# Kernel optimization log

Hardware: AMD Instinct MI355X
Metric: run time of the kernel (lower is better)

Reference implementation:

```python
import jax, jax.numpy as jnp
import numpy as np

EPS_INTERP = 1e-8
EPS_BN = 1e-5


def _bn_relu(x, gamma, beta):
    # x: [B, C, N]; training-mode BatchNorm1d over (B, N) with biased variance
    mean = jnp.mean(x, axis=(0, 2), keepdims=True)
    var = jnp.mean((x - mean) ** 2, axis=(0, 2), keepdims=True)
    xn = (x - mean) / jnp.sqrt(var + EPS_BN)
    return jax.nn.relu(xn * gamma[None, :, None] + beta[None, :, None])


def setup_inputs() -> dict:
    key = jax.random.key(0)
    ks = jax.random.split(key, 8)
    B, N, S, D = 16, 4096, 1024, 128
    return {
        "xyz1": jax.random.normal(ks[0], (B, 3, N), jnp.float32),
        "xyz2": jax.random.normal(ks[1], (B, 3, S), jnp.float32),
        "points1": jax.random.normal(ks[2], (B, D, N), jnp.float32),
        "points2": jax.random.normal(ks[3], (B, D, S), jnp.float32),
        "w0": jax.random.normal(ks[4], (256, 512), jnp.float32) * 0.04,
        "b0": jax.random.normal(ks[5], (256,), jnp.float32) * 0.01,
        "gamma0": jnp.ones((256,), jnp.float32),
        "beta0": jnp.zeros((256,), jnp.float32),
        "w1": jax.random.normal(ks[6], (128, 256), jnp.float32) * 0.06,
        "b1": jax.random.normal(ks[7], (128,), jnp.float32) * 0.01,
        "gamma1": jnp.ones((128,), jnp.float32),
        "beta1": jnp.zeros((128,), jnp.float32),
    }


def reference(xyz1, xyz2, points1, points2, w0, b0, gamma0, beta0, w1, b1, gamma1, beta1):
    # to [B, N, C] layouts
    x1 = jnp.transpose(xyz1, (0, 2, 1))   # [B, N, 3]
    x2 = jnp.transpose(xyz2, (0, 2, 1))   # [B, S, 3]
    p2 = jnp.transpose(points2, (0, 2, 1))  # [B, S, D]
    B, N, _ = x1.shape

    # squared pairwise distances [B, N, S]
    dists = (jnp.sum(x1 ** 2, -1)[:, :, None]
             + jnp.sum(x2 ** 2, -1)[:, None, :]
             - 2.0 * jnp.einsum('bnc,bsc->bns', x1, x2))

    # 3 nearest neighbors (ascending distance)
    neg_d, idx = jax.lax.top_k(-dists, 3)   # idx: [B, N, 3]
    d3 = -neg_d
    recip = 1.0 / (d3 + EPS_INTERP)
    weight = recip / jnp.sum(recip, axis=2, keepdims=True)  # [B, N, 3]

    # gather neighbor features: [B, N, 3, D]
    gathered = jax.vmap(lambda p, i: p[i])(p2, idx)
    # NOTE: this repo flattens the 3 weighted neighbors (no sum) -> [B, N, 3*D]
    interp = (gathered * weight[..., None]).reshape(B, N, -1)

    new_pts = jnp.concatenate([jnp.transpose(points1, (0, 2, 1)), interp], axis=-1)  # [B, N, 512]
    x = jnp.transpose(new_pts, (0, 2, 1))  # [B, 512, N]

    x = _bn_relu(jnp.einsum('oc,bcn->bon', w0, x) + b0[None, :, None], gamma0, beta0)
    x = _bn_relu(jnp.einsum('oc,bcn->bon', w1, x) + b1[None, :, None], gamma1, beta1)
    return x
```

## Files before the change

### kernel.cpp

```cpp
#include <hip/hip_runtime.h>
#include <stdint.h>

typedef unsigned short ushort_t;
typedef __attribute__((ext_vector_type(8))) __bf16 bf16x8;
typedef __attribute__((ext_vector_type(4))) float f32x4;

__device__ __forceinline__ float b2f(ushort_t u) {
    unsigned v = ((unsigned)u) << 16;
    float f;
    __builtin_memcpy(&f, &v, 4);
    return f;
}

__device__ __forceinline__ ushort_t f2b(float f) {
    __bf16 h = (__bf16)f;
    return __builtin_bit_cast(ushort_t, h);
}

__device__ __forceinline__ void gl_lds16(const void* g, void* l) {
    __builtin_amdgcn_global_load_lds((const __attribute__((address_space(1))) void*)g,
                                     (__attribute__((address_space(3))) void*)l, 16, 0, 0);
}

__global__ __launch_bounds__(256) void k_pre(const float* __restrict__ w0, ushort_t* __restrict__ w0b,
                                             const float* __restrict__ w1, ushort_t* __restrict__ w1b,
                                             const float* __restrict__ xyz2, float4* __restrict__ sdat,
                                             const float* __restrict__ points2, ushort_t* __restrict__ p2t,
                                             float* __restrict__ zb) {
    int bid = blockIdx.x;
    int t = threadIdx.x;
    if (bid < 512) {
        int i = bid * 256 + t;
        w0b[i] = f2b(w0[i]);
    } else if (bid < 640) {
        int i = (bid - 512) * 256 + t;
        w1b[i] = f2b(w1[i]);
    } else if (bid < 704) {
        int bb = bid - 640;
        int b = bb & 15, by = bb >> 4;
        int s = by * 256 + t;
        const float* x2 = xyz2 + (size_t)b * 3 * 1024;
        float x = x2[s], y = x2[1024 + s], z = x2[2048 + s];
        float4 v;
        v.x = x; v.y = y; v.z = z;
        v.w = __fadd_rn(__fadd_rn(__fmul_rn(x, x), __fmul_rn(y, y)), __fmul_rn(z, z));
        sdat[(size_t)b * 1024 + s] = v;
    } else if (bid < 960) {
        int bb = bid - 704;
        int b = bb & 15, sy = bb >> 4;
        int s = sy * 64 + (t & 63);
        int g = t >> 6;
        const float* src = points2 + (size_t)b * 128 * 1024 + s;
        ushort_t* dst = p2t + ((size_t)b * 1024 + s) * 128;
#pragma unroll
        for (int i = 0; i < 4; ++i) {
            int cp = i * 4 + g;
            ushort_t tmp[8];
#pragma unroll
            for (int k = 0; k < 8; ++k) tmp[k] = f2b(src[(size_t)(cp * 8 + k) * 1024]);
            *(uint4*)(dst + cp * 8) = *(const uint4*)tmp;
        }
    } else {
        zb[t] = 0.f; zb[256 + t] = 0.f;
        if (t < 128) { zb[512 + t] = 0.f; zb[640 + t] = 0.f; }
    }
}

__global__ __launch_bounds__(256) void k_interp(const float* __restrict__ xyz1,
                                                const float4* __restrict__ sdat,
                                                const float* __restrict__ points1,
                                                ushort_t* __restrict__ Xp1,
                                                int* __restrict__ sidxg,
                                                float* __restrict__ swg) {
    int b = blockIdx.x;
    int n0 = blockIdx.y * 32;
    int t = threadIdx.x;
    int tq = t & 31;
    int slice = t >> 5;
    int wave = t >> 6, lane = t & 63;

    __shared__ __align__(16) char sbuf[16384];
    float4* sP = (float4*)sbuf;
    __shared__ float sD[768];
    __shared__ int   sI[768];

    {
        const float4* src = sdat + (size_t)b * 1024;
#pragma unroll
        for (int c = 0; c < 4; ++c) {
            int p = wave * 256 + c * 64 + lane;
            gl_lds16(src + p, sbuf + p * 16);
        }
    }

    int n = n0 + tq;
    float x = xyz1[((size_t)b * 3 + 0) * 4096 + n];
    float y = xyz1[((size_t)b * 3 + 1) * 4096 + n];
    float z = xyz1[((size_t)b * 3 + 2) * 4096 + n];
    float s1 = __fadd_rn(__fadd_rn(__fmul_rn(x, x), __fmul_rn(y, y)), __fmul_rn(z, z));

    __syncthreads();

    const float* p1base = points1 + (size_t)b * 128 * 4096 + n0 + tq;
    float p1v[16];
#pragma unroll
    for (int i = 0; i < 2; ++i)
#pragma unroll
        for (int k = 0; k < 8; ++k)
            p1v[i * 8 + k] = p1base[(size_t)(((i * 8 + slice) * 8) + k) * 4096];

    float d0 = 1e30f, d1 = 1e30f, d2 = 1e30f;
    int i0 = 0, i1 = 0, i2 = 0;
    int sbeg = slice * 128;
    const float4* sdL = sP + sbeg;
#pragma unroll 8
    for (int s = 0; s < 128; ++s) {
        float4 v = sdL[s];
        float dot = fmaf(z, v.z, fmaf(y, v.y, __fmul_rn(x, v.x)));
        float d = __fadd_rn(fmaf(-2.0f, dot, s1), v.w);
        int si = sbeg + s;
        bool c0 = d < d0, c1 = d < d1, c2 = d < d2;
        i2 = c1 ? i1 : (c2 ? si : i2);
        i1 = c0 ? i0 : (c1 ? si : i1);
        i0 = c0 ? si : i0;
        d2 = fminf(fmaxf(d, d1), d2);
        d1 = fminf(fmaxf(d, d0), d1);
        d0 = fminf(d, d0);
    }
    sD[t * 3 + 0] = d0; sD[t * 3 + 1] = d1; sD[t * 3 + 2] = d2;
    sI[t * 3 + 0] = i0; sI[t * 3 + 1] = i1; sI[t * 3 + 2] = i2;

    {
        ushort_t* dstbase = Xp1 + (size_t)(b * 4096 + n0 + tq) * 128;
#pragma unroll
        for (int i = 0; i < 2; ++i) {
            int piece = i * 8 + slice;
            ushort_t tmp[8];
#pragma unroll
            for (int k = 0; k < 8; ++k) tmp[k] = f2b(p1v[i * 8 + k]);
            *(uint4*)(dstbase + piece * 8) = *(const uint4*)tmp;
        }
    }
    __syncthreads();

    if (t < 32) {
        int sel0 = -1, sel1 = -1;
        float seld[3]; int seli[3];
#pragma unroll
        for (int r = 0; r < 3; ++r) {
            float bd = 1e38f; int bi = 1 << 30;
            for (int k = 0; k < 24; ++k) {
                int s3 = (k * 0xAAAB) >> 17;
                int rank = k - s3 * 3;
                int base = (s3 * 32 + t) * 3 + rank;
                float cd = sD[base];
                int ci = sI[base];
                bool excl = (ci == sel0) | (ci == sel1);
                bool better = (!excl) & ((cd < bd) | ((cd == bd) & (ci < bi)));
                if (better) { bd = cd; bi = ci; }
            }
            seld[r] = bd; seli[r] = bi;
            if (r == 0) sel0 = bi; else if (r == 1) sel1 = bi;
        }
        float r0 = 1.0f / (seld[0] + 1e-8f);
        float r1 = 1.0f / (seld[1] + 1e-8f);
        float r2 = 1.0f / (seld[2] + 1e-8f);
        float rs = r0 + r1 + r2;
        size_t base = (size_t)(b * 4096 + n0 + t) * 3;
        sidxg[base + 0] = seli[0]; sidxg[base + 1] = seli[1]; sidxg[base + 2] = seli[2];
        swg[base + 0] = r0 / rs; swg[base + 1] = r1 / rs; swg[base + 2] = r2 / rs;
    }
}

__global__ __launch_bounds__(512, 4) void k_gemm(const ushort_t* __restrict__ A,
                                                 const ushort_t* __restrict__ Xp1,
                                                 const ushort_t* __restrict__ p2t,
                                                 const int* __restrict__ sidxg,
                                                 const float* __restrict__ swg,
                                                 const float* __restrict__ bias,
                                                 ushort_t* __restrict__ Y,
                                                 float* __restrict__ gs,
                                                 float* __restrict__ gq,
                                                 int Mtot, int K) {
    __shared__ __align__(16) char smem[54784];
    ushort_t* As = (ushort_t*)smem;
    ushort_t* Bs = (ushort_t*)(smem + 32768);
    ushort_t* sY = (ushort_t*)smem;
    float* red_s = (float*)(smem + 49152);
    float* red_q = red_s + 256;
    int*   lsi   = (int*)(smem + 51200);
    float* lsw   = (float*)(smem + 52736);

    int t = threadIdx.x;
    int j0 = blockIdx.x * 128;
    int b = j0 >> 12;
    int wave = t >> 6, lane = t & 63;
    int wm = wave >> 1, wn = wave & 1;
    int l16 = lane & 15, quad = lane >> 4;

    if (t < 256) { red_s[t] = 0.f; red_q[t] = 0.f; }
    if (t < 384) { lsi[t] = sidxg[(size_t)j0 * 3 + t]; lsw[t] = swg[(size_t)j0 * 3 + t]; }

    f32x4 acc[4][4] = {};

    int nk = K >> 6;
    for (int kt = 0; kt < nk; ++kt) {
#pragma unroll
        for (int c = 0; c < 4; ++c) {
            int idx = c * 512 + t;
            int row = idx >> 3, kc = idx & 7;
            gl_lds16(A + (size_t)row * K + kt * 64 + kc * 8, As + idx * 8);
        }
        if (kt < 2) {
#pragma unroll
            for (int c = 0; c < 2; ++c) {
                int idx = c * 512 + t;
                int row = idx >> 3, kc = idx & 7;
                gl_lds16(Xp1 + (size_t)(j0 + row) * 128 + kt * 64 + kc * 8, Bs + idx * 8);
            }
        } else {
            int r = (kt - 2) >> 1, h = (kt - 2) & 1;
#pragma unroll
            for (int c = 0; c < 2; ++c) {
                int idx = c * 512 + t;
                int row = idx >> 3, kc = idx & 7;
                int si = lsi[row * 3 + r];
                float w = lsw[row * 3 + r];
                const ushort_t* src = p2t + ((size_t)b * 1024 + si) * 128 + h * 64 + kc * 8;
                uint4 raw = *(const uint4*)src;
                ushort_t* e = (ushort_t*)&raw;
                ushort_t outv[8];
#pragma unroll
                for (int k = 0; k < 8; ++k) outv[k] = f2b(w * b2f(e[k]));
                *(uint4*)(Bs + idx * 8) = *(const uint4*)outv;
            }
        }
        __syncthreads();

#pragma unroll
        for (int kk = 0; kk < 2; ++kk) {
            bf16x8 af[4], bfr[4];
#pragma unroll
            for (int mi = 0; mi < 4; ++mi)
                af[mi] = *(const bf16x8*)(As + (wm * 64 + mi * 16 + l16) * 64 + kk * 32 + quad * 8);
#pragma unroll
            for (int ni = 0; ni < 4; ++ni)
                bfr[ni] = *(const bf16x8*)(Bs + (wn * 64 + ni * 16 + l16) * 64 + kk * 32 + quad * 8);
#pragma unroll
            for (int mi = 0; mi < 4; ++mi)
#pragma unroll
                for (int ni = 0; ni < 4; ++ni)
                    acc[mi][ni] = __builtin_amdgcn_mfma_f32_16x16x32_bf16(af[mi], bfr[ni], acc[mi][ni], 0, 0, 0);
        }
        __syncthreads();
    }

#pragma unroll
    for (int h = 0; h < 2; ++h) {
        if ((wm >> 1) == h) {
#pragma unroll
            for (int mi = 0; mi < 4; ++mi) {
                int obase = wm * 64 + mi * 16 + quad * 4;
                int ocol = obase - h * 128;
                float bv[4];
#pragma unroll
                for (int r = 0; r < 4; ++r) bv[r] = bias[obase + r];
                float sr[4] = {0.f, 0.f, 0.f, 0.f}, qr[4] = {0.f, 0.f, 0.f, 0.f};
#pragma unroll
                for (int ni = 0; ni < 4; ++ni) {
                    int j_local = wn * 64 + ni * 16 + l16;
                    ushort4 pk;
                    float v0 = acc[mi][ni][0] + bv[0];
                    float v1 = acc[mi][ni][1] + bv[1];
                    float v2 = acc[mi][ni][2] + bv[2];
                    float v3 = acc[mi][ni][3] + bv[3];
                    pk.x = f2b(v0); pk.y = f2b(v1); pk.z = f2b(v2); pk.w = f2b(v3);
                    sr[0] += v0; qr[0] += v0 * v0;
                    sr[1] += v1; qr[1] += v1 * v1;
                    sr[2] += v2; qr[2] += v2 * v2;
                    sr[3] += v3; qr[3] += v3 * v3;
                    *(ushort4*)(sY + j_local * 136 + ocol) = pk;
                }
#pragma unroll
                for (int r = 0; r < 4; ++r) {
                    float s = sr[r], q = qr[r];
                    s += __shfl_xor(s, 1); s += __shfl_xor(s, 2);
                    s += __shfl_xor(s, 4); s += __shfl_xor(s, 8);
                    q += __shfl_xor(q, 1); q += __shfl_xor(q, 2);
                    q += __shfl_xor(q, 4); q += __shfl_xor(q, 8);
                    if (l16 == 0) {
                        atomicAdd(&red_s[obase + r], s);
                        atomicAdd(&red_q[obase + r], q);
                    }
                }
            }
        }
        __syncthreads();
#pragma unroll
        for (int rep = 0; rep < 4; ++rep) {
            int idx = rep * 512 + t;
            int jl = idx >> 4;
            int o8 = idx & 15;
            uint4 vv = *(const uint4*)(sY + jl * 136 + o8 * 8);
            *(uint4*)(Y + (size_t)(j0 + jl) * Mtot + h * 128 + o8 * 8) = vv;
        }
        __syncthreads();
    }
    if (t < 256) {
        atomicAdd(&gs[t], red_s[t]);
        atomicAdd(&gq[t], red_q[t]);
    }
}

__global__ __launch_bounds__(256) void k_gemmf(const ushort_t* __restrict__ A,
                                               const ushort_t* __restrict__ Y0,
                                               const float* __restrict__ bias,
                                               const float* __restrict__ gamma0,
                                               const float* __restrict__ beta0,
                                               const float* __restrict__ gs0,
                                               const float* __restrict__ gq0,
                                               ushort_t* __restrict__ Y,
                                               float* __restrict__ gs1,
                                               float* __restrict__ gq1,
                                               int Mtot, int K) {
    __shared__ __align__(16) char smem[35840];
    ushort_t* As = (ushort_t*)smem;
    ushort_t* Bs = (ushort_t*)(smem + 16384);
    float* sa = (float*)(smem + 32768);
    float* sb = (float*)(smem + 33792);
    ushort_t* sY = (ushort_t*)smem;
    float* red_s = (float*)(smem + 34816);
    float* red_q = red_s + 128;

    int t = threadIdx.x;
    int m0 = blockIdx.x * 128;
    int j0 = blockIdx.y * 128;
    int wave = t >> 6, lane = t & 63;
    int wm = wave >> 1, wn = wave & 1;
    int l16 = lane & 15, quad = lane >> 4;

    {
        float s = gs0[t], q = gq0[t];
        float mean = s * (1.0f / 65536.0f);
        float var = q * (1.0f / 65536.0f) - mean * mean;
        float sc = gamma0[t] / sqrtf(var + 1e-5f);
        sa[t] = sc;
        sb[t] = beta0[t] - mean * sc;
    }
    if (t < 128) { red_s[t] = 0.f; red_q[t] = 0.f; }
    __syncthreads();

    f32x4 acc[4][4] = {};

    int nk = K >> 6;
    for (int kt = 0; kt < nk; ++kt) {
#pragma unroll
        for (int c = 0; c < 4; ++c) {
            int idx = c * 256 + t;
            int row = idx >> 3, kc = idx & 7;
            gl_lds16(A + (size_t)(m0 + row) * K + kt * 64 + kc * 8, As + idx * 8);
        }
#pragma unroll
        for (int c = 0; c < 4; ++c) {
            int idx = c * 256 + t;
            int row = idx >> 3, kc = idx & 7;
            int cbase = kt * 64 + kc * 8;
            uint4 raw = *(const uint4*)(Y0 + (size_t)(j0 + row) * K + cbase);
            ushort_t* e = (ushort_t*)&raw;
            ushort_t outv[8];
#pragma unroll
            for (int k = 0; k < 8; ++k) {
                float v = fmaxf(sa[cbase + k] * b2f(e[k]) + sb[cbase + k], 0.f);
                outv[k] = f2b(v);
            }
            *(uint4*)(Bs + idx * 8) = *(const uint4*)outv;
        }
        __syncthreads();

#pragma unroll
        for (int kk = 0; kk < 2; ++kk) {
            bf16x8 af[4], bfr[4];
#pragma unroll
            for (int mi = 0; mi < 4; ++mi)
                af[mi] = *(const bf16x8*)(As + (wm * 64 + mi * 16 + l16) * 64 + kk * 32 + quad * 8);
#pragma unroll
            for (int ni = 0; ni < 4; ++ni)
                bfr[ni] = *(const bf16x8*)(Bs + (wn * 64 + ni * 16 + l16) * 64 + kk * 32 + quad * 8);
#pragma unroll
            for (int mi = 0; mi < 4; ++mi)
#pragma unroll
                for (int ni = 0; ni < 4; ++ni)
                    acc[mi][ni] = __builtin_amdgcn_mfma_f32_16x16x32_bf16(af[mi], bfr[ni], acc[mi][ni], 0, 0, 0);
        }
        __syncthreads();
    }

#pragma unroll
    for (int mi = 0; mi < 4; ++mi) {
        int obase = wm * 64 + mi * 16 + quad * 4;
        float bv[4];
#pragma unroll
        for (int r = 0; r < 4; ++r) bv[r] = bias[m0 + obase + r];
        float sr[4] = {0.f, 0.f, 0.f, 0.f}, qr[4] = {0.f, 0.f, 0.f, 0.f};
#pragma unroll
        for (int ni = 0; ni < 4; ++ni) {
            int j_local = wn * 64 + ni * 16 + l16;
            ushort4 pk;
            float v0 = acc[mi][ni][0] + bv[0];
            float v1 = acc[mi][ni][1] + bv[1];
            float v2 = acc[mi][ni][2] + bv[2];
            float v3 = acc[mi][ni][3] + bv[3];
            pk.x = f2b(v0); pk.y = f2b(v1); pk.z = f2b(v2); pk.w = f2b(v3);
            sr[0] += v0; qr[0] += v0 * v0;
            sr[1] += v1; qr[1] += v1 * v1;
            sr[2] += v2; qr[2] += v2 * v2;
            sr[3] += v3; qr[3] += v3 * v3;
            *(ushort4*)(sY + j_local * 136 + obase) = pk;
        }
#pragma unroll
        for (int r = 0; r < 4; ++r) {
            float s = sr[r], q = qr[r];
            s += __shfl_xor(s, 1); s += __shfl_xor(s, 2);
            s += __shfl_xor(s, 4); s += __shfl_xor(s, 8);
            q += __shfl_xor(q, 1); q += __shfl_xor(q, 2);
            q += __shfl_xor(q, 4); q += __shfl_xor(q, 8);
            if (l16 == 0) {
                atomicAdd(&red_s[obase + r], s);
                atomicAdd(&red_q[obase + r], q);
            }
        }
    }
    __syncthreads();

#pragma unroll
    for (int rep = 0; rep < 8; ++rep) {
        int idx = rep * 256 + t;
        int jl = idx >> 4;
        int o8 = idx & 15;
        uint4 vv = *(const uint4*)(sY + jl * 136 + o8 * 8);
        *(uint4*)(Y + (size_t)(j0 + jl) * Mtot + m0 + o8 * 8) = vv;
    }
    if (t < 128) {
        atomicAdd(&gs1[m0 + t], red_s[t]);
        atomicAdd(&gq1[m0 + t], red_q[t]);
    }
}

__global__ __launch_bounds__(256) void k_out(const ushort_t* __restrict__ Y1,
                                             const float* __restrict__ gs1,
                                             const float* __restrict__ gq1,
                                             const float* __restrict__ gamma1,
                                             const float* __restrict__ beta1,
                                             float* __restrict__ out) {
    __shared__ float sa[128], sb[128];
    int t = threadIdx.x;
    if (t < 128) {
        float s = gs1[t], q = gq1[t];
        float mean = s * (1.0f / 65536.0f);
        float var = q * (1.0f / 65536.0f) - mean * mean;
        float sc = gamma1[t] / sqrtf(var + 1e-5f);
        sa[t] = sc;
        sb[t] = beta1[t] - mean * sc;
    }
    __syncthreads();
    int b = blockIdx.x;
    int nl = t & 127;
    int half = t >> 7;
    int n = blockIdx.y * 128 + nl;
    const uint4* src = (const uint4*)(Y1 + (size_t)(b * 4096 + n) * 128);
    float* dst = out + (size_t)b * 128 * 4096 + n;
    uint4 raw[8];
#pragma unroll
    for (int p = 0; p < 8; ++p) raw[p] = src[half * 8 + p];
    const ushort_t* e = (const ushort_t*)raw;
#pragma unroll
    for (int c = 0; c < 64; ++c) {
        int ch = half * 64 + c;
        float v = b2f(e[c]);
        v = fmaxf(sa[ch] * v + sb[ch], 0.f);
        dst[(size_t)ch * 4096] = v;
    }
}

extern "C" void kernel_launch(void* const* d_in, const int* in_sizes, int n_in,
                              void* d_out, int out_size, void* d_ws, size_t ws_size,
                              hipStream_t stream) {
    const float* xyz1    = (const float*)d_in[0];
    const float* xyz2    = (const float*)d_in[1];
    const float* points1 = (const float*)d_in[2];
    const float* points2 = (const float*)d_in[3];
    const float* w0      = (const float*)d_in[4];
    const float* b0      = (const float*)d_in[5];
    const float* gamma0  = (const float*)d_in[6];
    const float* beta0   = (const float*)d_in[7];
    const float* w1      = (const float*)d_in[8];
    const float* b1      = (const float*)d_in[9];
    const float* gamma1  = (const float*)d_in[10];
    const float* beta1   = (const float*)d_in[11];
    float* out = (float*)d_out;

    char* ws = (char*)d_ws;
    const size_t OFF_XP1  = 0;
    const size_t OFF_SIDX = 16777216;
    const size_t OFF_SW   = 17563648;
    const size_t OFF_Y0   = 67108864;
    const size_t OFF_Y1   = 100663296;
    const size_t OFF_P2T  = 117440512;
    const size_t OFF_W0B  = 121634816;
    const size_t OFF_W1B  = 121896960;
    const size_t OFF_AB   = 121962496;
    const size_t OFF_SDAT = 121965568;

    ushort_t* Xp1  = (ushort_t*)(ws + OFF_XP1);
    int*   sidxg   = (int*)(ws + OFF_SIDX);
    float* swg     = (float*)(ws + OFF_SW);
    ushort_t* Y0   = (ushort_t*)(ws + OFF_Y0);
    ushort_t* Y1   = (ushort_t*)(ws + OFF_Y1);
    ushort_t* p2t  = (ushort_t*)(ws + OFF_P2T);
    ushort_t* w0b  = (ushort_t*)(ws + OFF_W0B);
    ushort_t* w1b  = (ushort_t*)(ws + OFF_W1B);
    float* ab      = (float*)(ws + OFF_AB);
    float4* sdat   = (float4*)(ws + OFF_SDAT);
    float* gs0 = ab;        float* gq0 = ab + 256;
    float* gs1 = ab + 512;  float* gq1 = ab + 640;

    k_pre<<<961, 256, 0, stream>>>(w0, w0b, w1, w1b, xyz2, sdat, points2, p2t, ab);
    k_interp<<<dim3(16, 128), 256, 0, stream>>>(xyz1, sdat, points1, Xp1, sidxg, swg);
    k_gemm<<<512, 512, 0, stream>>>(w0b, Xp1, p2t, sidxg, swg, b0, Y0, gs0, gq0, 256, 512);
    k_gemmf<<<dim3(1, 512), 256, 0, stream>>>(w1b, Y0, b1, gamma0, beta0, gs0, gq0, Y1, gs1, gq1, 128, 256);
    k_out<<<dim3(16, 32), 256, 0, stream>>>(Y1, gs1, gq1, gamma1, beta1, out);
}
```

Before: 224.6 us.

## Split first GEMM into 128x128 tiles, swizzle LDS, prefetch neighbor gathers

The first fused GEMM moves from 256x128 output tiles with 512 threads to 128x128 tiles with 256 threads on a 2D grid, which doubles the block count and shrinks LDS use. Both GEMMs now use an XOR swizzle on LDS rows to avoid bank conflicts on the MFMA fragment loads. The gathered neighbor features for the next K-step are loaded into registers ahead of time so the global gather overlaps the current step's MFMAs. In exchange, the gather and weighting of interpolated features is repeated for each of the two M tiles, and register pressure rises.

Measured after the change: 236.0 us. +5.1%, slower.

```diff
diff --git a/kernel.cpp b/kernel.cpp
--- a/kernel.cpp
+++ b/kernel.cpp
@@ -172,7 +172,7 @@
     }
 }
 
-__global__ __launch_bounds__(512, 4) void k_gemm(const ushort_t* __restrict__ A,
+__global__ __launch_bounds__(256, 4) void k_gemm(const ushort_t* __restrict__ A,
                                                  const ushort_t* __restrict__ Xp1,
                                                  const ushort_t* __restrict__ p2t,
                                                  const int* __restrict__ sidxg,
@@ -182,57 +182,75 @@
                                                  float* __restrict__ gs,
                                                  float* __restrict__ gq,
                                                  int Mtot, int K) {
-    __shared__ __align__(16) char smem[54784];
+    __shared__ __align__(16) char smem[36864];
     ushort_t* As = (ushort_t*)smem;
-    ushort_t* Bs = (ushort_t*)(smem + 32768);
+    ushort_t* Bs = (ushort_t*)(smem + 16384);
+    int*   lsi   = (int*)(smem + 32768);
+    float* lsw   = (float*)(smem + 34304);
     ushort_t* sY = (ushort_t*)smem;
-    float* red_s = (float*)(smem + 49152);
-    float* red_q = red_s + 256;
-    int*   lsi   = (int*)(smem + 51200);
-    float* lsw   = (float*)(smem + 52736);
+    float* red_s = (float*)(smem + 35840);
+    float* red_q = red_s + 128;
 
     int t = threadIdx.x;
-    int j0 = blockIdx.x * 128;
-    int b = j0 >> 12;
+    int m0 = blockIdx.x * 128;
+    int j0 = blockIdx.y * 128;
+    int b = (j0 >> 12) & 15;
     int wave = t >> 6, lane = t & 63;
     int wm = wave >> 1, wn = wave & 1;
     int l16 = lane & 15, quad = lane >> 4;
-
-    if (t < 256) { red_s[t] = 0.f; red_q[t] = 0.f; }
-    if (t < 384) { lsi[t] = sidxg[(size_t)j0 * 3 + t]; lsw[t] = swg[(size_t)j0 * 3 + t]; }
+    int sw7 = l16 & 7;
+
+    if (t < 128) { red_s[t] = 0.f; red_q[t] = 0.f; }
+    for (int i = t; i < 384; i += 256) {
+        lsi[i] = sidxg[(size_t)j0 * 3 + i] & 1023;
+        lsw[i] = swg[(size_t)j0 * 3 + i];
+    }
 
     f32x4 acc[4][4] = {};
-
-    int nk = K >> 6;
-    for (int kt = 0; kt < nk; ++kt) {
+    uint4 bpreA[4], bpreB[4];
+    (void)K;
+
+#pragma unroll
+    for (int kt = 0; kt < 8; ++kt) {
 #pragma unroll
         for (int c = 0; c < 4; ++c) {
-            int idx = c * 512 + t;
+            int idx = c * 256 + t;
             int row = idx >> 3, kc = idx & 7;
-            gl_lds16(A + (size_t)row * K + kt * 64 + kc * 8, As + idx * 8);
+            gl_lds16(A + (size_t)(m0 + row) * 512 + kt * 64 + ((kc ^ (row & 7)) * 8),
+                     As + idx * 8);
         }
         if (kt < 2) {
 #pragma unroll
-            for (int c = 0; c < 2; ++c) {
-                int idx = c * 512 + t;
+            for (int c = 0; c < 4; ++c) {
+                int idx = c * 256 + t;
                 int row = idx >> 3, kc = idx & 7;
-                gl_lds16(Xp1 + (size_t)(j0 + row) * 128 + kt * 64 + kc * 8, Bs + idx * 8);
+                gl_lds16(Xp1 + (size_t)(j0 + row) * 128 + kt * 64 + ((kc ^ (row & 7)) * 8),
+                         Bs + idx * 8);
             }
         } else {
-            int r = (kt - 2) >> 1, h = (kt - 2) & 1;
-#pragma unroll
-            for (int c = 0; c < 2; ++c) {
-                int idx = c * 512 + t;
+            int r = (kt - 2) >> 1;
+#pragma unroll
+            for (int c = 0; c < 4; ++c) {
+                int idx = c * 256 + t;
                 int row = idx >> 3, kc = idx & 7;
-                int si = lsi[row * 3 + r];
                 float w = lsw[row * 3 + r];
-                const ushort_t* src = p2t + ((size_t)b * 1024 + si) * 128 + h * 64 + kc * 8;
-                uint4 raw = *(const uint4*)src;
+                uint4 raw = (kt & 1) ? bpreB[c] : bpreA[c];
                 ushort_t* e = (ushort_t*)&raw;
                 ushort_t outv[8];
 #pragma unroll
                 for (int k = 0; k < 8; ++k) outv[k] = f2b(w * b2f(e[k]));
-                *(uint4*)(Bs + idx * 8) = *(const uint4*)outv;
+                *(uint4*)(Bs + row * 64 + ((kc ^ (row & 7)) * 8)) = *(const uint4*)outv;
+            }
+        }
+        if (kt + 1 >= 2 && kt + 1 < 8) {
+            int rn = (kt - 1) >> 1, hn = (kt - 1) & 1;
+#pragma unroll
+            for (int c = 0; c < 4; ++c) {
+                int idx = c * 256 + t;
+                int row = idx >> 3, kc = idx & 7;
+                int si = lsi[row * 3 + rn] & 1023;
+                uint4 v = *(const uint4*)(p2t + (((size_t)b * 1024 + si) * 128) + hn * 64 + kc * 8);
+                if ((kt + 1) & 1) bpreB[c] = v; else bpreA[c] = v;
             }
         }
         __syncthreads();
@@ -242,10 +260,10 @@
             bf16x8 af[4], bfr[4];
 #pragma unroll
             for (int mi = 0; mi < 4; ++mi)
-                af[mi] = *(const bf16x8*)(As + (wm * 64 + mi * 16 + l16) * 64 + kk * 32 + quad * 8);
+                af[mi] = *(const bf16x8*)(As + (wm * 64 + mi * 16 + l16) * 64 + (((kk * 4 + quad) ^ sw7) * 8));
 #pragma unroll
             for (int ni = 0; ni < 4; ++ni)
-                bfr[ni] = *(const bf16x8*)(Bs + (wn * 64 + ni * 16 + l16) * 64 + kk * 32 + quad * 8);
+                bfr[ni] = *(const bf16x8*)(Bs + (wn * 64 + ni * 16 + l16) * 64 + (((kk * 4 + quad) ^ sw7) * 8));
 #pragma unroll
             for (int mi = 0; mi < 4; ++mi)
 #pragma unroll
@@ -256,59 +274,53 @@
     }
 
 #pragma unroll
-    for (int h = 0; h < 2; ++h) {
-        if ((wm >> 1) == h) {
-#pragma unroll
-            for (int mi = 0; mi < 4; ++mi) {
-                int obase = wm * 64 + mi * 16 + quad * 4;
-                int ocol = obase - h * 128;
-                float bv[4];
-#pragma unroll
-                for (int r = 0; r < 4; ++r) bv[r] = bias[obase + r];
-                float sr[4] = {0.f, 0.f, 0.f, 0.f}, qr[4] = {0.f, 0.f, 0.f, 0.f};
-#pragma unroll
-                for (int ni = 0; ni < 4; ++ni) {
-                    int j_local = wn * 64 + ni * 16 + l16;
-                    ushort4 pk;
-                    float v0 = acc[mi][ni][0] + bv[0];
-                    float v1 = acc[mi][ni][1] + bv[1];
-                    float v2 = acc[mi][ni][2] + bv[2];
-                    float v3 = acc[mi][ni][3] + bv[3];
-                    pk.x = f2b(v0); pk.y = f2b(v1); pk.z = f2b(v2); pk.w = f2b(v3);
-                    sr[0] += v0; qr[0] += v0 * v0;
-                    sr[1] += v1; qr[1] += v1 * v1;
-                    sr[2] += v2; qr[2] += v2 * v2;
-                    sr[3] += v3; qr[3] += v3 * v3;
-                    *(ushort4*)(sY + j_local * 136 + ocol) = pk;
-                }
-#pragma unroll
-                for (int r = 0; r < 4; ++r) {
-                    float s = sr[r], q = qr[r];
-                    s += __shfl_xor(s, 1); s += __shfl_xor(s, 2);
-                    s += __shfl_xor(s, 4); s += __shfl_xor(s, 8);
-                    q += __shfl_xor(q, 1); q += __shfl_xor(q, 2);
-                    q += __shfl_xor(q, 4); q += __shfl_xor(q, 8);
-                    if (l16 == 0) {
-                        atomicAdd(&red_s[obase + r], s);
-                        atomicAdd(&red_q[obase + r], q);
-                    }
-                }
-            }
-        }
-        __syncthreads();
-#pragma unroll
-        for (int rep = 0; rep < 4; ++rep) {
-            int idx = rep * 512 + t;
-            int jl = idx >> 4;
-            int o8 = idx & 15;
-            uint4 vv = *(const uint4*)(sY + jl * 136 + o8 * 8);
-            *(uint4*)(Y + (size_t)(j0 + jl) * Mtot + h * 128 + o8 * 8) = vv;
-        }
-        __syncthreads();
-    }
-    if (t < 256) {
-        atomicAdd(&gs[t], red_s[t]);
-        atomicAdd(&gq[t], red_q[t]);
+    for (int mi = 0; mi < 4; ++mi) {
+        int obase = wm * 64 + mi * 16 + quad * 4;
+        float bv[4];
+#pragma unroll
+        for (int r = 0; r < 4; ++r) bv[r] = bias[m0 + obase + r];
+        float sr[4] = {0.f, 0.f, 0.f, 0.f}, qr[4] = {0.f, 0.f, 0.f, 0.f};
+#pragma unroll
+        for (int ni = 0; ni < 4; ++ni) {
+            int j_local = wn * 64 + ni * 16 + l16;
+            ushort4 pk;
+            float v0 = acc[mi][ni][0] + bv[0];
+            float v1 = acc[mi][ni][1] + bv[1];
+            float v2 = acc[mi][ni][2] + bv[2];
+            float v3 = acc[mi][ni][3] + bv[3];
+            pk.x = f2b(v0); pk.y = f2b(v1); pk.z = f2b(v2); pk.w = f2b(v3);
+            sr[0] += v0; qr[0] += v0 * v0;
+            sr[1] += v1; qr[1] += v1 * v1;
+            sr[2] += v2; qr[2] += v2 * v2;
+            sr[3] += v3; qr[3] += v3 * v3;
+            *(ushort4*)(sY + j_local * 136 + obase) = pk;
+        }
+#pragma unroll
+        for (int r = 0; r < 4; ++r) {
+            float s = sr[r], q = qr[r];
+            s += __shfl_xor(s, 1); s += __shfl_xor(s, 2);
+            s += __shfl_xor(s, 4); s += __shfl_xor(s, 8);
+            q += __shfl_xor(q, 1); q += __shfl_xor(q, 2);
+            q += __shfl_xor(q, 4); q += __shfl_xor(q, 8);
+            if (l16 == 0) {
+                atomicAdd(&red_s[obase + r], s);
+                atomicAdd(&red_q[obase + r], q);
+            }
+        }
+    }
+    __syncthreads();
+
+#pragma unroll
+    for (int rep = 0; rep < 8; ++rep) {
+        int idx = rep * 256 + t;
+        int jl = idx >> 4;
+        int o8 = idx & 15;
+        uint4 vv = *(const uint4*)(sY + jl * 136 + o8 * 8);
+        *(uint4*)(Y + (size_t)(j0 + jl) * Mtot + m0 + o8 * 8) = vv;
+    }
+    if (t < 128) {
+        atomicAdd(&gs[m0 + t], red_s[t]);
+        atomicAdd(&gq[m0 + t], red_q[t]);
     }
 }
 
@@ -338,6 +350,7 @@
     int wave = t >> 6, lane = t & 63;
     int wm = wave >> 1, wn = wave & 1;
     int l16 = lane & 15, quad = lane >> 4;
+    int sw7 = l16 & 7;
 
     {
         float s = gs0[t], q = gq0[t];
@@ -358,7 +371,7 @@
         for (int c = 0; c < 4; ++c) {
             int idx = c * 256 + t;
             int row = idx >> 3, kc = idx & 7;
-            gl_lds16(A + (size_t)(m0 + row) * K + kt * 64 + kc * 8, As + idx * 8);
+            gl_lds16(A + (size_t)(m0 + row) * K + kt * 64 + ((kc ^ (row & 7)) * 8), As + idx * 8);
         }
 #pragma unroll
         for (int c = 0; c < 4; ++c) {
@@ -373,7 +386,7 @@
                 float v = fmaxf(sa[cbase + k] * b2f(e[k]) + sb[cbase + k], 0.f);
                 outv[k] = f2b(v);
             }
-            *(uint4*)(Bs + idx * 8) = *(const uint4*)outv;
+            *(uint4*)(Bs + row * 64 + ((kc ^ (row & 7)) * 8)) = *(const uint4*)outv;
         }
         __syncthreads();
 
@@ -382,10 +395,10 @@
             bf16x8 af[4], bfr[4];
 #pragma unroll
             for (int mi = 0; mi < 4; ++mi)
-                af[mi] = *(const bf16x8*)(As + (wm * 64 + mi * 16 + l16) * 64 + kk * 32 + quad * 8);
+                af[mi] = *(const bf16x8*)(As + (wm * 64 + mi * 16 + l16) * 64 + (((kk * 4 + quad) ^ sw7) * 8));
 #pragma unroll
             for (int ni = 0; ni < 4; ++ni)
-                bfr[ni] = *(const bf16x8*)(Bs + (wn * 64 + ni * 16 + l16) * 64 + kk * 32 + quad * 8);
+                bfr[ni] = *(const bf16x8*)(Bs + (wn * 64 + ni * 16 + l16) * 64 + (((kk * 4 + quad) ^ sw7) * 8));
 #pragma unroll
             for (int mi = 0; mi < 4; ++mi)
 #pragma unroll
@@ -526,7 +539,7 @@
 
     k_pre<<<961, 256, 0, stream>>>(w0, w0b, w1, w1b, xyz2, sdat, points2, p2t, ab);
     k_interp<<<dim3(16, 128), 256, 0, stream>>>(xyz1, sdat, points1, Xp1, sidxg, swg);
-    k_gemm<<<512, 512, 0, stream>>>(w0b, Xp1, p2t, sidxg, swg, b0, Y0, gs0, gq0, 256, 512);
+    k_gemm<<<dim3(2, 512), 256, 0, stream>>>(w0b, Xp1, p2t, sidxg, swg, b0, Y0, gs0, gq0, 256, 512);
     k_gemmf<<<dim3(1, 512), 256, 0, stream>>>(w1b, Y0, b1, gamma0, beta0, gs0, gq0, Y1, gs1, gq1, 128, 256);
     k_out<<<dim3(16, 32), 256, 0, stream>>>(Y1, gs1, gq1, gamma1, beta1, out);
 }
```

## Materialize full concat input in interp kernel and XOR-swizzle GEMM LDS tiles

Applied to the files above, without the earlier changes.

The interp kernel now gathers and weights the three neighbor feature rows itself and writes a full 512-wide bf16 activation row. The first GEMM can then load its B operand with async global-to-LDS copies instead of doing register gathers inside the K loop. Both GEMMs also XOR-swizzle the LDS tile layout to avoid bank conflicts on the MFMA fragment reads. The cost is a larger intermediate buffer written and re-read through global memory (512 instead of 128 columns per point).

New measurement: 218.6 us. 2.7% less time.

```diff
diff --git a/kernel.cpp b/kernel.cpp
--- a/kernel.cpp
+++ b/kernel.cpp
@@ -69,9 +69,8 @@
 __global__ __launch_bounds__(256) void k_interp(const float* __restrict__ xyz1,
                                                 const float4* __restrict__ sdat,
                                                 const float* __restrict__ points1,
-                                                ushort_t* __restrict__ Xp1,
-                                                int* __restrict__ sidxg,
-                                                float* __restrict__ swg) {
+                                                const ushort_t* __restrict__ p2t,
+                                                ushort_t* __restrict__ X) {
     int b = blockIdx.x;
     int n0 = blockIdx.y * 32;
     int t = threadIdx.x;
@@ -81,6 +80,8 @@
 
     __shared__ __align__(16) char sbuf[16384];
     float4* sP = (float4*)sbuf;
+    int*   sidx = (int*)sbuf;
+    float* sw   = (float*)(sbuf + 384);
     __shared__ float sD[768];
     __shared__ int   sI[768];
 
@@ -131,7 +132,7 @@
     sI[t * 3 + 0] = i0; sI[t * 3 + 1] = i1; sI[t * 3 + 2] = i2;
 
     {
-        ushort_t* dstbase = Xp1 + (size_t)(b * 4096 + n0 + tq) * 128;
+        ushort_t* dstbase = X + (size_t)(b * 4096 + n0 + tq) * 512;
 #pragma unroll
         for (int i = 0; i < 2; ++i) {
             int piece = i * 8 + slice;
@@ -166,40 +167,53 @@
         float r1 = 1.0f / (seld[1] + 1e-8f);
         float r2 = 1.0f / (seld[2] + 1e-8f);
         float rs = r0 + r1 + r2;
-        size_t base = (size_t)(b * 4096 + n0 + t) * 3;
-        sidxg[base + 0] = seli[0]; sidxg[base + 1] = seli[1]; sidxg[base + 2] = seli[2];
-        swg[base + 0] = r0 / rs; swg[base + 1] = r1 / rs; swg[base + 2] = r2 / rs;
+        sw[t * 3 + 0] = r0 / rs; sw[t * 3 + 1] = r1 / rs; sw[t * 3 + 2] = r2 / rs;
+        sidx[t * 3 + 0] = seli[0]; sidx[t * 3 + 1] = seli[1]; sidx[t * 3 + 2] = seli[2];
+    }
+    __syncthreads();
+
+#pragma unroll
+    for (int i = 0; i < 6; ++i) {
+        int idx = i * 256 + t;
+        int q = idx / 48;
+        int rem = idx - q * 48;
+        int r = rem >> 4;
+        int piece = rem & 15;
+        int si = sidx[q * 3 + r] & 1023;
+        float wt = sw[q * 3 + r];
+        const ushort_t* src = p2t + ((size_t)b * 1024 + si) * 128 + piece * 8;
+        uint4 raw = *(const uint4*)src;
+        ushort_t* e = (ushort_t*)&raw;
+        ushort_t outv[8];
+#pragma unroll
+        for (int k = 0; k < 8; ++k) outv[k] = f2b(wt * b2f(e[k]));
+        ushort_t* dst = X + (size_t)(b * 4096 + n0 + q) * 512 + 128 + r * 128 + piece * 8;
+        *(uint4*)dst = *(const uint4*)outv;
     }
 }
 
 __global__ __launch_bounds__(512, 4) void k_gemm(const ushort_t* __restrict__ A,
-                                                 const ushort_t* __restrict__ Xp1,
-                                                 const ushort_t* __restrict__ p2t,
-                                                 const int* __restrict__ sidxg,
-                                                 const float* __restrict__ swg,
+                                                 const ushort_t* __restrict__ Bt,
                                                  const float* __restrict__ bias,
                                                  ushort_t* __restrict__ Y,
                                                  float* __restrict__ gs,
                                                  float* __restrict__ gq,
                                                  int Mtot, int K) {
-    __shared__ __align__(16) char smem[54784];
+    __shared__ __align__(16) char smem[51200];
     ushort_t* As = (ushort_t*)smem;
     ushort_t* Bs = (ushort_t*)(smem + 32768);
     ushort_t* sY = (ushort_t*)smem;
     float* red_s = (float*)(smem + 49152);
     float* red_q = red_s + 256;
-    int*   lsi   = (int*)(smem + 51200);
-    float* lsw   = (float*)(smem + 52736);
 
     int t = threadIdx.x;
     int j0 = blockIdx.x * 128;
-    int b = j0 >> 12;
     int wave = t >> 6, lane = t & 63;
     int wm = wave >> 1, wn = wave & 1;
     int l16 = lane & 15, quad = lane >> 4;
+    int sw7 = l16 & 7;
 
     if (t < 256) { red_s[t] = 0.f; red_q[t] = 0.f; }
-    if (t < 384) { lsi[t] = sidxg[(size_t)j0 * 3 + t]; lsw[t] = swg[(size_t)j0 * 3 + t]; }
 
     f32x4 acc[4][4] = {};
 
@@ -209,31 +223,13 @@
         for (int c = 0; c < 4; ++c) {
             int idx = c * 512 + t;
             int row = idx >> 3, kc = idx & 7;
-            gl_lds16(A + (size_t)row * K + kt * 64 + kc * 8, As + idx * 8);
-        }
-        if (kt < 2) {
-#pragma unroll
-            for (int c = 0; c < 2; ++c) {
-                int idx = c * 512 + t;
-                int row = idx >> 3, kc = idx & 7;
-                gl_lds16(Xp1 + (size_t)(j0 + row) * 128 + kt * 64 + kc * 8, Bs + idx * 8);
-            }
-        } else {
-            int r = (kt - 2) >> 1, h = (kt - 2) & 1;
-#pragma unroll
-            for (int c = 0; c < 2; ++c) {
-                int idx = c * 512 + t;
-                int row = idx >> 3, kc = idx & 7;
-                int si = lsi[row * 3 + r];
-                float w = lsw[row * 3 + r];
-                const ushort_t* src = p2t + ((size_t)b * 1024 + si) * 128 + h * 64 + kc * 8;
-                uint4 raw = *(const uint4*)src;
-                ushort_t* e = (ushort_t*)&raw;
-                ushort_t outv[8];
-#pragma unroll
-                for (int k = 0; k < 8; ++k) outv[k] = f2b(w * b2f(e[k]));
-                *(uint4*)(Bs + idx * 8) = *(const uint4*)outv;
-            }
+            gl_lds16(A + (size_t)row * K + kt * 64 + ((kc ^ (row & 7)) * 8), As + idx * 8);
+        }
+#pragma unroll
+        for (int c = 0; c < 2; ++c) {
+            int idx = c * 512 + t;
+            int row = idx >> 3, kc = idx & 7;
+            gl_lds16(Bt + (size_t)(j0 + row) * K + kt * 64 + ((kc ^ (row & 7)) * 8), Bs + idx * 8);
         }
         __syncthreads();
 
@@ -242,10 +238,10 @@
             bf16x8 af[4], bfr[4];
 #pragma unroll
             for (int mi = 0; mi < 4; ++mi)
-                af[mi] = *(const bf16x8*)(As + (wm * 64 + mi * 16 + l16) * 64 + kk * 32 + quad * 8);
+                af[mi] = *(const bf16x8*)(As + (wm * 64 + mi * 16 + l16) * 64 + (((kk * 4 + quad) ^ sw7) * 8));
 #pragma unroll
             for (int ni = 0; ni < 4; ++ni)
-                bfr[ni] = *(const bf16x8*)(Bs + (wn * 64 + ni * 16 + l16) * 64 + kk * 32 + quad * 8);
+                bfr[ni] = *(const bf16x8*)(Bs + (wn * 64 + ni * 16 + l16) * 64 + (((kk * 4 + quad) ^ sw7) * 8));
 #pragma unroll
             for (int mi = 0; mi < 4; ++mi)
 #pragma unroll
@@ -338,6 +334,7 @@
     int wave = t >> 6, lane = t & 63;
     int wm = wave >> 1, wn = wave & 1;
     int l16 = lane & 15, quad = lane >> 4;
+    int sw7 = l16 & 7;
 
     {
         float s = gs0[t], q = gq0[t];
@@ -358,7 +355,7 @@
         for (int c = 0; c < 4; ++c) {
             int idx = c * 256 + t;
             int row = idx >> 3, kc = idx & 7;
-            gl_lds16(A + (size_t)(m0 + row) * K + kt * 64 + kc * 8, As + idx * 8);
+            gl_lds16(A + (size_t)(m0 + row) * K + kt * 64 + ((kc ^ (row & 7)) * 8), As + idx * 8);
         }
 #pragma unroll
         for (int c = 0; c < 4; ++c) {
@@ -373,7 +370,7 @@
                 float v = fmaxf(sa[cbase + k] * b2f(e[k]) + sb[cbase + k], 0.f);
                 outv[k] = f2b(v);
             }
-            *(uint4*)(Bs + idx * 8) = *(const uint4*)outv;
+            *(uint4*)(Bs + row * 64 + ((kc ^ (row & 7)) * 8)) = *(const uint4*)outv;
         }
         __syncthreads();
 
@@ -382,10 +379,10 @@
             bf16x8 af[4], bfr[4];
 #pragma unroll
             for (int mi = 0; mi < 4; ++mi)
-                af[mi] = *(const bf16x8*)(As + (wm * 64 + mi * 16 + l16) * 64 + kk * 32 + quad * 8);
+                af[mi] = *(const bf16x8*)(As + (wm * 64 + mi * 16 + l16) * 64 + (((kk * 4 + quad) ^ sw7) * 8));
 #pragma unroll
             for (int ni = 0; ni < 4; ++ni)
-                bfr[ni] = *(const bf16x8*)(Bs + (wn * 64 + ni * 16 + l16) * 64 + kk * 32 + quad * 8);
+                bfr[ni] = *(const bf16x8*)(Bs + (wn * 64 + ni * 16 + l16) * 64 + (((kk * 4 + quad) ^ sw7) * 8));
 #pragma unroll
             for (int mi = 0; mi < 4; ++mi)
 #pragma unroll
@@ -500,9 +497,7 @@
     float* out = (float*)d_out;
 
     char* ws = (char*)d_ws;
-    const size_t OFF_XP1  = 0;
-    const size_t OFF_SIDX = 16777216;
-    const size_t OFF_SW   = 17563648;
+    const size_t OFF_X    = 0;
     const size_t OFF_Y0   = 67108864;
     const size_t OFF_Y1   = 100663296;
     const size_t OFF_P2T  = 117440512;
@@ -511,9 +506,7 @@
     const size_t OFF_AB   = 121962496;
     const size_t OFF_SDAT = 121965568;
 
-    ushort_t* Xp1  = (ushort_t*)(ws + OFF_XP1);
-    int*   sidxg   = (int*)(ws + OFF_SIDX);
-    float* swg     = (float*)(ws + OFF_SW);
+    ushort_t* X    = (ushort_t*)(ws + OFF_X);
     ushort_t* Y0   = (ushort_t*)(ws + OFF_Y0);
     ushort_t* Y1   = (ushort_t*)(ws + OFF_Y1);
     ushort_t* p2t  = (ushort_t*)(ws + OFF_P2T);
@@ -525,8 +518,8 @@
     float* gs1 = ab + 512;  float* gq1 = ab + 640;
 
     k_pre<<<961, 256, 0, stream>>>(w0, w0b, w1, w1b, xyz2, sdat, points2, p2t, ab);
-    k_interp<<<dim3(16, 128), 256, 0, stream>>>(xyz1, sdat, points1, Xp1, sidxg, swg);
-    k_gemm<<<512, 512, 0, stream>>>(w0b, Xp1, p2t, sidxg, swg, b0, Y0, gs0, gq0, 256, 512);
+    k_interp<<<dim3(16, 128), 256, 0, stream>>>(xyz1, sdat, points1, p2t, X);
+    k_gemm<<<512, 512, 0, stream>>>(w0b, X, b0, Y0, gs0, gq0, 256, 512);
     k_gemmf<<<dim3(1, 512), 256, 0, stream>>>(w1b, Y0, b1, gamma0, beta0, gs0, gq0, Y1, gs1, gq1, 128, 256);
     k_out<<<dim3(16, 32), 256, 0, stream>>>(Y1, gs1, gq1, gamma1, beta1, out);
 }
```
